# Performance work log

Measured on AMD Instinct MI355X. Metric: run time of the kernel, lower is better.

The kernel has to match this reference:

```python
import jax, jax.numpy as jnp
import numpy as np
from jax import lax

B = 4096
SRC = 50   # source_seq_len (encoder runs SRC-1 steps)
TGT = 25   # target_seq_len
R = 1024   # rnn_size
H = 67     # HUMAN_SIZE
I = 82     # input_size = 67 + 15 one-hot actions


def gru_cell(x, h, Wi, Wh, bi, bh):
    # torch.nn.GRUCell semantics; gate order (r, z, n); Wi:[3R,in], Wh:[3R,R]
    gi = x @ Wi.T + bi
    gh = h @ Wh.T + bh
    ir, iz, inn = jnp.split(gi, 3, axis=1)
    hr, hz, hn = jnp.split(gh, 3, axis=1)
    r = jax.nn.sigmoid(ir + hr)
    z = jax.nn.sigmoid(iz + hz)
    n = jnp.tanh(inn + r * hn)
    return (1.0 - z) * n + z * h


def setup_inputs() -> dict:
    key = jax.random.key(0)
    ks = jax.random.split(key, 12)
    s = 0.05
    return {
        "encoder_inputs": jax.random.normal(ks[0], (B, SRC - 1, I), jnp.float32),
        "decoder_inputs": jax.random.normal(ks[1], (B, TGT, I), jnp.float32),
        "Wi1": jax.random.normal(ks[2], (3 * R, I), jnp.float32) * s,
        "Wh1": jax.random.normal(ks[3], (3 * R, R), jnp.float32) * s,
        "bi1": jax.random.normal(ks[4], (3 * R,), jnp.float32) * s,
        "bh1": jax.random.normal(ks[5], (3 * R,), jnp.float32) * s,
        "Wi2": jax.random.normal(ks[6], (3 * R, R), jnp.float32) * s,
        "Wh2": jax.random.normal(ks[7], (3 * R, R), jnp.float32) * s,
        "bi2": jax.random.normal(ks[8], (3 * R,), jnp.float32) * s,
        "bh2": jax.random.normal(ks[9], (3 * R,), jnp.float32) * s,
        "Wfc": jax.random.normal(ks[10], (H, 2 * R), jnp.float32) * s,
        "bfc": jax.random.normal(ks[11], (H,), jnp.float32) * s,
        "use_cuda": 0,
    }


def reference(encoder_inputs, decoder_inputs, Wi1, Wh1, bi1, bh1,
              Wi2, Wh2, bi2, bh2, Wfc, bfc, use_cuda):
    # dropout=0.0 / eval mode -> dropout is identity (faithful to module defaults)
    bsz = encoder_inputs.shape[0]
    enc = jnp.transpose(encoder_inputs, (1, 0, 2))  # [SRC-1, B, I]
    dec = jnp.transpose(decoder_inputs, (1, 0, 2))  # [TGT,   B, I]

    s1 = jnp.zeros((bsz, R), encoder_inputs.dtype)
    s2 = jnp.zeros((bsz, R), encoder_inputs.dtype)

    def enc_step(carry, x):
        s1, s2 = carry
        s1 = gru_cell(x, s1, Wi1, Wh1, bi1, bh1)
        s2 = gru_cell(s1, s2, Wi2, Wh2, bi2, bh2)
        return (s1, s2), None

    (s1, s2), _ = lax.scan(enc_step, (s1, s2), enc)

    # decoder feeds back previous output (loop_function = identity on prev)
    prev0 = dec[0][:, :H]

    def dec_step(carry, dec_t):
        s1, s2, prev = carry
        inp = lax.stop_gradient(jnp.concatenate([prev, dec_t[:, H:]], axis=1))  # .detach()
        s1 = gru_cell(inp, s1, Wi1, Wh1, bi1, bh1)
        s2 = gru_cell(s1, s2, Wi2, Wh2, bi2, bh2)
        state_out = jnp.concatenate([s1, s2], axis=1)          # [B, 2R]
        out = inp[:, :H] + state_out @ Wfc.T + bfc             # residual velocities
        return (s1, s2, out), out

    _, outputs = lax.scan(dec_step, (s1, s2, prev0), dec)      # [TGT, B, H]
    return jnp.transpose(outputs, (1, 0, 2))                   # [B, TGT, H]
```

## Files before the change

kernel.cpp:

```cpp
#include <hip/hip_runtime.h>
#include <hip/hip_bf16.h>
#include <math.h>

#define B_        4096
#define ENC_STEPS 49
#define TGT_      25
#define R_        1024
#define H_        67
#define I_        82
#define IP_       96
#define IP2_      192
#define NG_       3072
#define FCN_      128
#define K2_       2048

typedef unsigned short u16;
typedef __attribute__((ext_vector_type(8))) short bf16x8_t;
typedef __attribute__((ext_vector_type(4))) float f32x4_t;

__device__ __forceinline__ float bf2f(u16 h) {
    union { unsigned int u; float f; } v; v.u = ((unsigned int)h) << 16; return v.f;
}
__device__ __forceinline__ u16 f2bf(float f) {
    union { unsigned int u; float f; } v; v.f = f;
    unsigned int u = v.u;
    u += 0x7fffu + ((u >> 16) & 1u);
    return (u16)(u >> 16);
}
__device__ __forceinline__ float sigmf(float x) { return 1.f / (1.f + __expf(-x)); }
__device__ __forceinline__ float tanhfast(float x) { return 1.f - 2.f / (__expf(2.f * x) + 1.f); }

__device__ __forceinline__ void g2l16(const u16* g, u16* l) {
    __builtin_amdgcn_global_load_lds(
        (const __attribute__((address_space(1))) unsigned int*)(const void*)g,
        (__attribute__((address_space(3))) unsigned int*)(void*)l,
        16, 0, 0);
}

__global__ void cast_bf16_kernel(const float* __restrict__ s, u16* __restrict__ d, int n) {
    int i = blockIdx.x * 256 + threadIdx.x;
    if (i < n) d[i] = f2bf(s[i]);
}
__global__ void pad_wi1_dup_kernel(const float* __restrict__ s, u16* __restrict__ d) {
    int i = blockIdx.x * 256 + threadIdx.x;
    if (i >= NG_ * IP2_) return;
    int r = i / IP2_, c = i % IP2_;
    int cc = (c < IP_) ? c : c - IP_;
    d[i] = (cc < I_) ? f2bf(s[r * I_ + cc]) : (u16)0;
}
__global__ void pad_wfc_kernel(const float* __restrict__ s, u16* __restrict__ d) {
    int i = blockIdx.x * 256 + threadIdx.x;
    if (i >= FCN_ * K2_) return;
    int r = i / K2_, c = i % K2_;
    d[i] = (r < H_) ? f2bf(s[r * K2_ + c]) : (u16)0;
}

__global__ void pad_all_x_kernel(const float* __restrict__ enc, u16* __restrict__ xall) {
    int i = blockIdx.x * 256 + threadIdx.x;
    if (i >= B_ * ENC_STEPS * IP_) return;
    int c = i % IP_;
    int t = (i / IP_) % ENC_STEPS;
    int b = i / (IP_ * ENC_STEPS);
    float v = (c < I_) ? enc[((size_t)b * ENC_STEPS + t) * I_ + c] : 0.f;
    u16 hi = f2bf(v);
    u16 lo = f2bf(v - bf2f(hi));
    size_t base = ((size_t)t * B_ + b) * IP2_;
    xall[base + c]       = hi;
    xall[base + IP_ + c] = lo;
}

__global__ void build_inp_kernel(const float* __restrict__ prev, int pstride,
                                 const float* __restrict__ dec, int t,
                                 u16* __restrict__ xpad) {
    int i = blockIdx.x * 256 + threadIdx.x;
    if (i >= B_ * IP_) return;
    int b = i / IP_, c = i % IP_;
    float v = 0.f;
    if (c < H_)      v = prev[(size_t)b * pstride + c];
    else if (c < I_) v = dec[((size_t)b * TGT_ + t) * I_ + c];
    u16 hi = f2bf(v);
    u16 lo = f2bf(v - bf2f(hi));
    xpad[(size_t)b * IP2_ + c]       = hi;
    xpad[(size_t)b * IP2_ + IP_ + c] = lo;
}

template<int KX>
__global__ __launch_bounds__(256, 2) void gru_step_kernel(
    const u16* __restrict__ Ax, int ldax,
    const u16* __restrict__ Wx,
    const u16* __restrict__ Ah, int ldah,
    const u16* __restrict__ Wh,
    const float* __restrict__ bi, const float* __restrict__ bh,
    float* __restrict__ hf,
    u16* __restrict__ hout)
{
    __shared__ __align__(16) u16 As[128 * 32];
    __shared__ __align__(16) u16 Ws[3 * 64 * 32];

    const int tid  = threadIdx.x;
    const int lane = tid & 63, wave = tid >> 6;
    const int wm = wave >> 1, wn = wave & 1;
    const int mbase = blockIdx.y * 128;
    const int nbase = blockIdx.x * 64;
    const int lr = lane & 15, lk = (lane >> 4) * 8;

    f32x4_t acc_r[4][2], acc_z[4][2], acc_xn[4][2], acc_hn[4][2];
#pragma unroll
    for (int i = 0; i < 4; i++)
#pragma unroll
        for (int j = 0; j < 2; j++) {
            acc_r[i][j]  = (f32x4_t){0,0,0,0};
            acc_z[i][j]  = (f32x4_t){0,0,0,0};
            acc_xn[i][j] = (f32x4_t){0,0,0,0};
            acc_hn[i][j] = (f32x4_t){0,0,0,0};
        }

    for (int k0 = 0; k0 < KX; k0 += 32) {
        __syncthreads();
#pragma unroll
        for (int p = 0; p < 2; p++) {
            int g = tid + p * 256;
            g2l16(Ax + (size_t)(mbase + (g >> 2)) * ldax + k0 + (g & 3) * 8, As + g * 8);
        }
#pragma unroll
        for (int p = 0; p < 3; p++) {
            int q = tid + p * 256;
            int gate = q >> 8, rg = (q >> 2) & 63, cw = q & 3;
            g2l16(Wx + ((size_t)gate * R_ + nbase + rg) * KX + k0 + cw * 8, Ws + q * 8);
        }
        __syncthreads();
        bf16x8_t a_f[4], w_r[2], w_z[2], w_n[2];
#pragma unroll
        for (int i = 0; i < 4; i++)
            a_f[i] = *(const bf16x8_t*)(As + (wm * 64 + i * 16 + lr) * 32 + lk);
#pragma unroll
        for (int j = 0; j < 2; j++) {
            int c = wn * 32 + j * 16 + lr;
            w_r[j] = *(const bf16x8_t*)(Ws + c * 32 + lk);
            w_z[j] = *(const bf16x8_t*)(Ws + (64 + c) * 32 + lk);
            w_n[j] = *(const bf16x8_t*)(Ws + (128 + c) * 32 + lk);
        }
#pragma unroll
        for (int i = 0; i < 4; i++)
#pragma unroll
            for (int j = 0; j < 2; j++) {
                acc_r[i][j]  = __builtin_amdgcn_mfma_f32_16x16x32_bf16(a_f[i], w_r[j], acc_r[i][j], 0, 0, 0);
                acc_z[i][j]  = __builtin_amdgcn_mfma_f32_16x16x32_bf16(a_f[i], w_z[j], acc_z[i][j], 0, 0, 0);
                acc_xn[i][j] = __builtin_amdgcn_mfma_f32_16x16x32_bf16(a_f[i], w_n[j], acc_xn[i][j], 0, 0, 0);
            }
    }

    for (int k0 = 0; k0 < R_; k0 += 32) {
        __syncthreads();
#pragma unroll
        for (int p = 0; p < 2; p++) {
            int g = tid + p * 256;
            g2l16(Ah + (size_t)(mbase + (g >> 2)) * ldah + k0 + (g & 3) * 8, As + g * 8);
        }
#pragma unroll
        for (int p = 0; p < 3; p++) {
            int q = tid + p * 256;
            int gate = q >> 8, rg = (q >> 2) & 63, cw = q & 3;
            g2l16(Wh + ((size_t)gate * R_ + nbase + rg) * R_ + k0 + cw * 8, Ws + q * 8);
        }
        __syncthreads();
        bf16x8_t a_f[4], w_r[2], w_z[2], w_n[2];
#pragma unroll
        for (int i = 0; i < 4; i++)
            a_f[i] = *(const bf16x8_t*)(As + (wm * 64 + i * 16 + lr) * 32 + lk);
#pragma unroll
        for (int j = 0; j < 2; j++) {
            int c = wn * 32 + j * 16 + lr;
            w_r[j] = *(const bf16x8_t*)(Ws + c * 32 + lk);
            w_z[j] = *(const bf16x8_t*)(Ws + (64 + c) * 32 + lk);
            w_n[j] = *(const bf16x8_t*)(Ws + (128 + c) * 32 + lk);
        }
#pragma unroll
        for (int i = 0; i < 4; i++)
#pragma unroll
            for (int j = 0; j < 2; j++) {
                acc_r[i][j]  = __builtin_amdgcn_mfma_f32_16x16x32_bf16(a_f[i], w_r[j], acc_r[i][j], 0, 0, 0);
                acc_z[i][j]  = __builtin_amdgcn_mfma_f32_16x16x32_bf16(a_f[i], w_z[j], acc_z[i][j], 0, 0, 0);
                acc_hn[i][j] = __builtin_amdgcn_mfma_f32_16x16x32_bf16(a_f[i], w_n[j], acc_hn[i][j], 0, 0, 0);
            }
    }

    const int rr2 = (lane >> 4) * 4;
#pragma unroll
    for (int j = 0; j < 2; j++) {
        const int col = nbase + wn * 32 + j * 16 + lr;
        const float b_ir = bi[col],          b_hr = bh[col];
        const float b_iz = bi[R_ + col],     b_hz = bh[R_ + col];
        const float b_in = bi[2 * R_ + col], b_hn = bh[2 * R_ + col];
#pragma unroll
        for (int i = 0; i < 4; i++) {
#pragma unroll
            for (int r = 0; r < 4; r++) {
                const int row = mbase + wm * 64 + i * 16 + rr2 + r;
                const float hold = hf[(size_t)row * R_ + col];
                const float rv = sigmf(acc_r[i][j][r] + b_ir + b_hr);
                const float zv = sigmf(acc_z[i][j][r] + b_iz + b_hz);
                const float nv = tanhfast(acc_xn[i][j][r] + b_in + rv * (acc_hn[i][j][r] + b_hn));
                const float hn = (1.f - zv) * nv + zv * hold;
                hf[(size_t)row * R_ + col] = hn;
                hout[(size_t)row * K2_ + col] = f2bf(hn);
            }
        }
    }
}

__global__ __launch_bounds__(256) void fc_part_kernel(
    const u16* __restrict__ A, const u16* __restrict__ W, float* __restrict__ part) {
    __shared__ __align__(16) u16 As[64 * 32];
    __shared__ __align__(16) u16 Bs[128 * 32];
    const int tid  = threadIdx.x;
    const int lane = tid & 63, wave = tid >> 6;
    const int wm = wave >> 1, wn = wave & 1;
    const int mbase = blockIdx.y * 64;
    const int kbase = blockIdx.x * 512;
    const int lr = lane & 15, lk = (lane >> 4) * 8;

    f32x4_t acc[2][4];
#pragma unroll
    for (int i = 0; i < 2; i++)
#pragma unroll
        for (int j = 0; j < 4; j++) acc[i][j] = (f32x4_t){0, 0, 0, 0};

    for (int k0 = 0; k0 < 512; k0 += 32) {
        __syncthreads();
        {
            int g = tid;
            g2l16(A + (size_t)(mbase + (g >> 2)) * K2_ + kbase + k0 + (g & 3) * 8, As + g * 8);
        }
#pragma unroll
        for (int p = 0; p < 2; p++) {
            int q = tid + p * 256;
            g2l16(W + (size_t)(q >> 2) * K2_ + kbase + k0 + (q & 3) * 8, Bs + q * 8);
        }
        __syncthreads();
        bf16x8_t a_f[2], b_f[4];
#pragma unroll
        for (int i = 0; i < 2; i++)
            a_f[i] = *(const bf16x8_t*)(As + (wm * 32 + i * 16 + lr) * 32 + lk);
#pragma unroll
        for (int j = 0; j < 4; j++)
            b_f[j] = *(const bf16x8_t*)(Bs + (wn * 64 + j * 16 + lr) * 32 + lk);
#pragma unroll
        for (int i = 0; i < 2; i++)
#pragma unroll
            for (int j = 0; j < 4; j++)
                acc[i][j] = __builtin_amdgcn_mfma_f32_16x16x32_bf16(a_f[i], b_f[j], acc[i][j], 0, 0, 0);
    }
    const int rr2 = (lane >> 4) * 4;
#pragma unroll
    for (int i = 0; i < 2; i++)
#pragma unroll
        for (int r = 0; r < 4; r++) {
            int row = mbase + wm * 32 + i * 16 + rr2 + r;
#pragma unroll
            for (int j = 0; j < 4; j++) {
                int col = wn * 64 + j * 16 + lr;
                part[((size_t)blockIdx.x * B_ + row) * FCN_ + col] = acc[i][j][r];
            }
        }
}

__global__ void fc_finish_kernel(const float* __restrict__ part, const float* __restrict__ prev,
                                 int pstride, const float* __restrict__ bfc,
                                 float* __restrict__ out, int t) {
    int i = blockIdx.x * 256 + threadIdx.x;
    if (i >= B_ * H_) return;
    int b = i / H_, c = i % H_;
    size_t idx = (size_t)b * FCN_ + c;
    const size_t S = (size_t)B_ * FCN_;
    float s = (part[idx] + part[S + idx]) + (part[2 * S + idx] + part[3 * S + idx]);
    out[((size_t)b * TGT_ + t) * H_ + c] = prev[(size_t)b * pstride + c] + s + bfc[c];
}

extern "C" void kernel_launch(void* const* d_in, const int* in_sizes, int n_in,
                              void* d_out, int out_size, void* d_ws, size_t ws_size,
                              hipStream_t stream) {
    (void)in_sizes; (void)n_in; (void)out_size; (void)ws_size;
    const float* enc = (const float*)d_in[0];
    const float* dec = (const float*)d_in[1];
    const float* Wi1 = (const float*)d_in[2];
    const float* Wh1 = (const float*)d_in[3];
    const float* bi1 = (const float*)d_in[4];
    const float* bh1 = (const float*)d_in[5];
    const float* Wi2 = (const float*)d_in[6];
    const float* Wh2 = (const float*)d_in[7];
    const float* bi2 = (const float*)d_in[8];
    const float* bh2 = (const float*)d_in[9];
    const float* Wfc = (const float*)d_in[10];
    const float* bfc = (const float*)d_in[11];
    float* out = (float*)d_out;

    char* ws = (char*)d_ws;
    size_t off = 0;
    auto alloc = [&](size_t bytes) -> char* {
        char* p = ws + off;
        off += (bytes + 255) & ~(size_t)255;
        return p;
    };
    u16* Wh1b  = (u16*)alloc((size_t)NG_ * R_ * 2);
    u16* Wi2b  = (u16*)alloc((size_t)NG_ * R_ * 2);
    u16* Wh2b  = (u16*)alloc((size_t)NG_ * R_ * 2);
    u16* Wi1pb = (u16*)alloc((size_t)NG_ * IP2_ * 2);
    u16* Wfcb  = (u16*)alloc((size_t)FCN_ * K2_ * 2);
    u16* sbuf0 = (u16*)alloc((size_t)B_ * K2_ * 2);
    float* s1f = (float*)alloc((size_t)B_ * R_ * 4);
    float* s2f = (float*)alloc((size_t)B_ * R_ * 4);
    u16* sbuf1 = (u16*)alloc((size_t)B_ * K2_ * 2);
    u16* xall  = (u16*)alloc((size_t)ENC_STEPS * B_ * IP2_ * 2);
    u16* xpad2 = (u16*)alloc((size_t)B_ * IP2_ * 2);
    float* cfcp = (float*)alloc((size_t)4 * B_ * FCN_ * 4);
    u16* sbuf[2] = { sbuf0, sbuf1 };

    hipMemsetAsync(sbuf0, 0,
                   (size_t)B_ * K2_ * 2 + 2 * (size_t)B_ * R_ * 4, stream);

    cast_bf16_kernel<<<(NG_ * R_ + 255) / 256, 256, 0, stream>>>(Wh1, Wh1b, NG_ * R_);
    cast_bf16_kernel<<<(NG_ * R_ + 255) / 256, 256, 0, stream>>>(Wi2, Wi2b, NG_ * R_);
    cast_bf16_kernel<<<(NG_ * R_ + 255) / 256, 256, 0, stream>>>(Wh2, Wh2b, NG_ * R_);
    pad_wi1_dup_kernel<<<(NG_ * IP2_ + 255) / 256, 256, 0, stream>>>(Wi1, Wi1pb);
    pad_wfc_kernel<<<(FCN_ * K2_ + 255) / 256, 256, 0, stream>>>(Wfc, Wfcb);
    pad_all_x_kernel<<<(B_ * ENC_STEPS * IP_ + 255) / 256, 256, 0, stream>>>(enc, xall);

    dim3 gru_grid(R_ / 64, B_ / 128, 1);
    dim3 fc_grid(4, B_ / 64, 1);
    const int binp_blocks = (B_ * IP_ + 255) / 256;
    const int fcf_blocks  = (B_ * H_ + 255) / 256;

    int phase = 0;

    for (int t = 0; t < ENC_STEPS; t++) {
        u16* cur = sbuf[phase];
        u16* nxt = sbuf[phase ^ 1];
        gru_step_kernel<IP2_><<<gru_grid, 256, 0, stream>>>(
            xall + (size_t)t * B_ * IP2_, IP2_, Wi1pb,
            cur, K2_, Wh1b, bi1, bh1, s1f, nxt);
        gru_step_kernel<R_><<<gru_grid, 256, 0, stream>>>(
            nxt, K2_, Wi2b,
            cur + R_, K2_, Wh2b, bi2, bh2, s2f, nxt + R_);
        phase ^= 1;
    }

    for (int t = 0; t < TGT_; t++) {
        const float* prev;
        int pstride;
        if (t == 0) { prev = dec;                 pstride = TGT_ * I_; }
        else        { prev = out + (t - 1) * H_;  pstride = TGT_ * H_; }
        u16* cur = sbuf[phase];
        u16* nxt = sbuf[phase ^ 1];
        build_inp_kernel<<<binp_blocks, 256, 0, stream>>>(prev, pstride, dec, t, xpad2);
        gru_step_kernel<IP2_><<<gru_grid, 256, 0, stream>>>(
            xpad2, IP2_, Wi1pb,
            cur, K2_, Wh1b, bi1, bh1, s1f, nxt);
        gru_step_kernel<R_><<<gru_grid, 256, 0, stream>>>(
            nxt, K2_, Wi2b,
            cur + R_, K2_, Wh2b, bi2, bh2, s2f, nxt + R_);
        fc_part_kernel<<<fc_grid, 256, 0, stream>>>(nxt, Wfcb, cfcp);
        fc_finish_kernel<<<fcf_blocks, 256, 0, stream>>>(cfcp, prev, pstride, bfc, out, t);
        phase ^= 1;
    }
}
```

Baseline: 8.640 ms.

## Double-buffer GRU step LDS tiles, reorder LDS layout, remap block order

The GRU step kernel merges its input and hidden K-loops into one loop over double-buffered LDS tiles, loading the next tile while MFMAs run on the current one, which cuts one barrier per iteration. Both the GRU and FC kernels switch to a k-chunk-major LDS layout, meant to avoid bank conflicts on the 16-byte fragment reads. Block indices are also remapped so neighbouring blocks share N tiles, aiming for better L2 reuse of weights. The cost is twice the LDS per block, which may limit occupancy.

```diff
diff --git a/kernel.cpp b/kernel.cpp
--- a/kernel.cpp
+++ b/kernel.cpp
@@ -94,15 +94,23 @@
     float* __restrict__ hf,
     u16* __restrict__ hout)
 {
-    __shared__ __align__(16) u16 As[128 * 32];
-    __shared__ __align__(16) u16 Ws[3 * 64 * 32];
+    constexpr int NX = KX / 32;
+    constexpr int NH = R_ / 32;
+    constexpr int NT = NX + NH;
+
+    __shared__ __align__(16) u16 As[2 * 512 * 8];
+    __shared__ __align__(16) u16 Ws[2 * 768 * 8];
 
     const int tid  = threadIdx.x;
     const int lane = tid & 63, wave = tid >> 6;
     const int wm = wave >> 1, wn = wave & 1;
-    const int mbase = blockIdx.y * 128;
-    const int nbase = blockIdx.x * 64;
-    const int lr = lane & 15, lk = (lane >> 4) * 8;
+    const int lin = blockIdx.x + gridDim.x * blockIdx.y;
+    const int nb  = ((lin & 7) << 1) | ((lin >> 3) & 1);
+    const int mb  = lin >> 4;
+    const int mbase = mb * 128;
+    const int nbase = nb * 64;
+    const int lr = lane & 15;
+    const int kc = lane >> 4;
 
     f32x4_t acc_r[4][2], acc_z[4][2], acc_xn[4][2], acc_hn[4][2];
 #pragma unroll
@@ -115,74 +123,68 @@
             acc_hn[i][j] = (f32x4_t){0,0,0,0};
         }
 
-    for (int k0 = 0; k0 < KX; k0 += 32) {
-        __syncthreads();
+    auto stage = [&](int it, int buf) {
+        const u16* Asrc; int lda; const u16* Wsrc; int wk; int k0;
+        if (it < NX) { Asrc = Ax; lda = ldax; Wsrc = Wx; wk = KX; k0 = it * 32; }
+        else         { Asrc = Ah; lda = ldah; Wsrc = Wh; wk = R_; k0 = (it - NX) * 32; }
+        u16* ab = As + buf * 4096;
+        u16* wb = Ws + buf * 6144;
 #pragma unroll
         for (int p = 0; p < 2; p++) {
             int g = tid + p * 256;
-            g2l16(Ax + (size_t)(mbase + (g >> 2)) * ldax + k0 + (g & 3) * 8, As + g * 8);
+            int kch = g >> 7, row = g & 127;
+            g2l16(Asrc + (size_t)(mbase + row) * lda + k0 + kch * 8, ab + g * 8);
         }
 #pragma unroll
         for (int p = 0; p < 3; p++) {
             int q = tid + p * 256;
-            int gate = q >> 8, rg = (q >> 2) & 63, cw = q & 3;
-            g2l16(Wx + ((size_t)gate * R_ + nbase + rg) * KX + k0 + cw * 8, Ws + q * 8);
-        }
+            int kch = q / 192, row = q % 192;
+            int gate = row >> 6, rg = row & 63;
+            g2l16(Wsrc + ((size_t)gate * R_ + nbase + rg) * wk + k0 + kch * 8, wb + q * 8);
+        }
+    };
+
+    auto compute = [&](int it, int buf) {
+        const u16* ab = As + buf * 4096;
+        const u16* wb = Ws + buf * 6144;
+        bf16x8_t a_f[4], w_r[2], w_z[2], w_n[2];
+#pragma unroll
+        for (int i = 0; i < 4; i++)
+            a_f[i] = *(const bf16x8_t*)(ab + (kc * 128 + wm * 64 + i * 16 + lr) * 8);
+#pragma unroll
+        for (int j = 0; j < 2; j++) {
+            int rw = wn * 32 + j * 16 + lr;
+            w_r[j] = *(const bf16x8_t*)(wb + (kc * 192 + rw) * 8);
+            w_z[j] = *(const bf16x8_t*)(wb + (kc * 192 + 64 + rw) * 8);
+            w_n[j] = *(const bf16x8_t*)(wb + (kc * 192 + 128 + rw) * 8);
+        }
+        if (it < NX) {
+#pragma unroll
+            for (int i = 0; i < 4; i++)
+#pragma unroll
+                for (int j = 0; j < 2; j++) {
+                    acc_r[i][j]  = __builtin_amdgcn_mfma_f32_16x16x32_bf16(a_f[i], w_r[j], acc_r[i][j], 0, 0, 0);
+                    acc_z[i][j]  = __builtin_amdgcn_mfma_f32_16x16x32_bf16(a_f[i], w_z[j], acc_z[i][j], 0, 0, 0);
+                    acc_xn[i][j] = __builtin_amdgcn_mfma_f32_16x16x32_bf16(a_f[i], w_n[j], acc_xn[i][j], 0, 0, 0);
+                }
+        } else {
+#pragma unroll
+            for (int i = 0; i < 4; i++)
+#pragma unroll
+                for (int j = 0; j < 2; j++) {
+                    acc_r[i][j]  = __builtin_amdgcn_mfma_f32_16x16x32_bf16(a_f[i], w_r[j], acc_r[i][j], 0, 0, 0);
+                    acc_z[i][j]  = __builtin_amdgcn_mfma_f32_16x16x32_bf16(a_f[i], w_z[j], acc_z[i][j], 0, 0, 0);
+                    acc_hn[i][j] = __builtin_amdgcn_mfma_f32_16x16x32_bf16(a_f[i], w_n[j], acc_hn[i][j], 0, 0, 0);
+                }
+        }
+    };
+
+    stage(0, 0);
+    for (int it = 0; it < NT; it++) {
+        int buf = it & 1;
         __syncthreads();
-        bf16x8_t a_f[4], w_r[2], w_z[2], w_n[2];
-#pragma unroll
-        for (int i = 0; i < 4; i++)
-            a_f[i] = *(const bf16x8_t*)(As + (wm * 64 + i * 16 + lr) * 32 + lk);
-#pragma unroll
-        for (int j = 0; j < 2; j++) {
-            int c = wn * 32 + j * 16 + lr;
-            w_r[j] = *(const bf16x8_t*)(Ws + c * 32 + lk);
-            w_z[j] = *(const bf16x8_t*)(Ws + (64 + c) * 32 + lk);
-            w_n[j] = *(const bf16x8_t*)(Ws + (128 + c) * 32 + lk);
-        }
-#pragma unroll
-        for (int i = 0; i < 4; i++)
-#pragma unroll
-            for (int j = 0; j < 2; j++) {
-                acc_r[i][j]  = __builtin_amdgcn_mfma_f32_16x16x32_bf16(a_f[i], w_r[j], acc_r[i][j], 0, 0, 0);
-                acc_z[i][j]  = __builtin_amdgcn_mfma_f32_16x16x32_bf16(a_f[i], w_z[j], acc_z[i][j], 0, 0, 0);
-                acc_xn[i][j] = __builtin_amdgcn_mfma_f32_16x16x32_bf16(a_f[i], w_n[j], acc_xn[i][j], 0, 0, 0);
-            }
-    }
-
-    for (int k0 = 0; k0 < R_; k0 += 32) {
-        __syncthreads();
-#pragma unroll
-        for (int p = 0; p < 2; p++) {
-            int g = tid + p * 256;
-            g2l16(Ah + (size_t)(mbase + (g >> 2)) * ldah + k0 + (g & 3) * 8, As + g * 8);
-        }
-#pragma unroll
-        for (int p = 0; p < 3; p++) {
-            int q = tid + p * 256;
-            int gate = q >> 8, rg = (q >> 2) & 63, cw = q & 3;
-            g2l16(Wh + ((size_t)gate * R_ + nbase + rg) * R_ + k0 + cw * 8, Ws + q * 8);
-        }
-        __syncthreads();
-        bf16x8_t a_f[4], w_r[2], w_z[2], w_n[2];
-#pragma unroll
-        for (int i = 0; i < 4; i++)
-            a_f[i] = *(const bf16x8_t*)(As + (wm * 64 + i * 16 + lr) * 32 + lk);
-#pragma unroll
-        for (int j = 0; j < 2; j++) {
-            int c = wn * 32 + j * 16 + lr;
-            w_r[j] = *(const bf16x8_t*)(Ws + c * 32 + lk);
-            w_z[j] = *(const bf16x8_t*)(Ws + (64 + c) * 32 + lk);
-            w_n[j] = *(const bf16x8_t*)(Ws + (128 + c) * 32 + lk);
-        }
-#pragma unroll
-        for (int i = 0; i < 4; i++)
-#pragma unroll
-            for (int j = 0; j < 2; j++) {
-                acc_r[i][j]  = __builtin_amdgcn_mfma_f32_16x16x32_bf16(a_f[i], w_r[j], acc_r[i][j], 0, 0, 0);
-                acc_z[i][j]  = __builtin_amdgcn_mfma_f32_16x16x32_bf16(a_f[i], w_z[j], acc_z[i][j], 0, 0, 0);
-                acc_hn[i][j] = __builtin_amdgcn_mfma_f32_16x16x32_bf16(a_f[i], w_n[j], acc_hn[i][j], 0, 0, 0);
-            }
+        if (it + 1 < NT) stage(it + 1, buf ^ 1);
+        compute(it, buf);
     }
 
     const int rr2 = (lane >> 4) * 4;
@@ -218,7 +220,7 @@
     const int wm = wave >> 1, wn = wave & 1;
     const int mbase = blockIdx.y * 64;
     const int kbase = blockIdx.x * 512;
-    const int lr = lane & 15, lk = (lane >> 4) * 8;
+    const int lr = lane & 15, kc = lane >> 4;
 
     f32x4_t acc[2][4];
 #pragma unroll
@@ -230,21 +232,23 @@
         __syncthreads();
         {
             int g = tid;
-            g2l16(A + (size_t)(mbase + (g >> 2)) * K2_ + kbase + k0 + (g & 3) * 8, As + g * 8);
+            int kch = g >> 6, row = g & 63;
+            g2l16(A + (size_t)(mbase + row) * K2_ + kbase + k0 + kch * 8, As + g * 8);
         }
 #pragma unroll
         for (int p = 0; p < 2; p++) {
             int q = tid + p * 256;
-            g2l16(W + (size_t)(q >> 2) * K2_ + kbase + k0 + (q & 3) * 8, Bs + q * 8);
+            int kch = q >> 7, row = q & 127;
+            g2l16(W + (size_t)row * K2_ + kbase + k0 + kch * 8, Bs + q * 8);
         }
         __syncthreads();
         bf16x8_t a_f[2], b_f[4];
 #pragma unroll
         for (int i = 0; i < 2; i++)
-            a_f[i] = *(const bf16x8_t*)(As + (wm * 32 + i * 16 + lr) * 32 + lk);
+            a_f[i] = *(const bf16x8_t*)(As + (kc * 64 + wm * 32 + i * 16 + lr) * 8);
 #pragma unroll
         for (int j = 0; j < 4; j++)
-            b_f[j] = *(const bf16x8_t*)(Bs + (wn * 64 + j * 16 + lr) * 32 + lk);
+            b_f[j] = *(const bf16x8_t*)(Bs + (kc * 128 + wn * 64 + j * 16 + lr) * 8);
 #pragma unroll
         for (int i = 0; i < 2; i++)
 #pragma unroll
@@ -326,7 +330,7 @@
     pad_wfc_kernel<<<(FCN_ * K2_ + 255) / 256, 256, 0, stream>>>(Wfc, Wfcb);
     pad_all_x_kernel<<<(B_ * ENC_STEPS * IP_ + 255) / 256, 256, 0, stream>>>(enc, xall);
 
-    dim3 gru_grid(R_ / 64, B_ / 128, 1);
+    dim3 gru_grid(16, 32, 1);
     dim3 fc_grid(4, B_ / 64, 1);
     const int binp_blocks = (B_ * IP_ + 255) / 256;
     const int fcf_blocks  = (B_ * H_ + 255) / 256;
```

Result: slower. 24.55 ms (+184.2%).
